# Kernel optimization log

Measured on AMD Instinct MI355X. Metric: run time of the kernel, lower is better.

The kernel has to match this reference:

```python
import jax, jax.numpy as jnp
import numpy as np

N_NODES = 100_000
N_EDGES = 6_400_000  # avg degree 64
ONE_THIRD = 1.0 / 3.0


def _safe_cbrt(x):
    # x >= 0 by construction (relu upstream); guard x==0 so pow grad stays finite.
    pos = x > 0
    xs = jnp.where(pos, x, 1.0)
    return jnp.where(pos, xs ** ONE_THIRD, 0.0)


def setup_inputs() -> dict:
    key = jax.random.key(0)
    ks = jax.random.split(key, 8)
    T = jax.random.uniform(ks[0], (N_NODES,), jnp.float32, 1.8, 4.5)          # node temperature [K]
    cp = jax.random.uniform(ks[1], (N_NODES,), jnp.float32, 0.5, 2.0)         # node thermal capacity
    L = jax.random.uniform(ks[2], (N_EDGES,), jnp.float32, 0.1, 2.0)          # edge length (>0)
    conductivity = jax.random.uniform(ks[3], (N_EDGES,), jnp.float32, 0.5, 1.5)
    A = jax.random.uniform(ks[4], (N_EDGES,), jnp.float32, 0.01, 1.0)         # cross-section area
    src = jax.random.randint(ks[5], (N_EDGES,), 0, N_NODES, jnp.int32)
    dst = jax.random.randint(ks[6], (N_EDGES,), 0, N_NODES, jnp.int32)
    time_step = jnp.full((1,), 0.1, jnp.float32)                              # context scalar
    return {"T": T, "cp": cp, "L": L, "conductivity": conductivity, "A": A,
            "time_step": time_step, "src": src, "dst": dst}


def reference(T, cp, L, conductivity, A, time_step, src, dst):
    n = T.shape[0]
    # broadcast node -> edge; relu(-(T_target - T_source)) == relu(T_src - T_dst)
    delta_T = jax.nn.relu(T[src] - T[dst])                 # [E]
    gradient_T = delta_T / L                               # [E]
    heat_flux_density = _safe_cbrt(gradient_T * conductivity)
    heat_flux = heat_flux_density * A
    E_transf_conduction = heat_flux * time_step            # broadcast [1]
    cp_s = cp[src]
    cp_t = cp[dst]
    combined_cp = cp_t * cp_s / (cp_t + cp_s)
    max_energy = delta_T * combined_cp
    E_transf = jnp.minimum(E_transf_conduction, max_energy)
    heat_sent = jax.ops.segment_sum(E_transf, src, num_segments=n)
    heat_received = jax.ops.segment_sum(E_transf, dst, num_segments=n)
    return heat_received - heat_sent                       # [N]
```

## Files before the change

### kernel.cpp

```cpp
#include <hip/hip_runtime.h>
#include <hip/hip_bf16.h>
#include <hip/hip_fp16.h>

#define NRANGE   8
#define RLEN_MAX 12800
#define N_XCD    8
#define SL_XCD   8
#define SLICES   64
#define WIN_E    2048

typedef float vfloat4 __attribute__((ext_vector_type(4)));
typedef unsigned long long u64;

__global__ void __launch_bounds__(256)
pack_nodes_kernel(const float* __restrict__ T, const float* __restrict__ cp,
                  float2* __restrict__ nodes, int* __restrict__ tails, int n) {
    int i = blockIdx.x * blockDim.x + threadIdx.x;
    if (i < n) nodes[i] = make_float2(T[i], cp[i]);
    if (blockIdx.x == 0 && threadIdx.x < SLICES) tails[threadIdx.x] = 0;
}

__device__ __forceinline__ float edge_e(float2 ns, float2 nd, float Li,
                                        float ci, float Ai, float dt) {
    const float delta = ns.x - nd.x;
    if (delta <= 0.0f) return 0.0f;
    const float x = (delta / Li) * ci;
    const float ec = cbrtf(x) * Ai * dt;
    const float comb = (nd.y * ns.y) / (nd.y + ns.y);
    return fminf(ec, delta * comb);
}

__device__ __forceinline__ u64 make_rec(int s, int d, float e) {
    return (u64)(unsigned)s | ((u64)(unsigned)d << 17)
         | ((u64)__half_as_ushort(__float2half_rn(e)) << 34);
}

__global__ void __launch_bounds__(512)
etrec_kernel(const float2* __restrict__ nodes,
             const float* __restrict__ L,
             const float* __restrict__ cond,
             const float* __restrict__ A,
             const float* __restrict__ time_step,
             const int* __restrict__ src,
             const int* __restrict__ dst,
             u64* __restrict__ recs,
             int* __restrict__ tails,
             int n_edges, int wps, int cap) {
    __shared__ u64 srec[8 * 256];
    __shared__ int wcnt[8];
    __shared__ int wbase[8];
    __shared__ int sbase;

    const int wpx  = SL_XCD * wps;
    const int w    = (blockIdx.x % N_XCD) * wpx + blockIdx.x / N_XCD;
    const int s    = w / wps;
    const int e0   = w * WIN_E;
    const int wave = threadIdx.x >> 6;
    const int lane = threadIdx.x & 63;

    int my_off = 0;
    const bool active = (e0 < n_edges);

    if (active) {
        const float dt = time_step[0];
        float ev[4]; int sv[4]; int dv[4];

        if (e0 + WIN_E <= n_edges) {
            const int kk = (e0 >> 2) + threadIdx.x;
            const int4    si = ((const int4*)src)[kk];
            const int4    di = ((const int4*)dst)[kk];
            const vfloat4 Lv = __builtin_nontemporal_load(&((const vfloat4*)L)[kk]);
            const vfloat4 cv = __builtin_nontemporal_load(&((const vfloat4*)cond)[kk]);
            const vfloat4 Av = __builtin_nontemporal_load(&((const vfloat4*)A)[kk]);
            const float2 ns0 = nodes[si.x], ns1 = nodes[si.y], ns2 = nodes[si.z], ns3 = nodes[si.w];
            const float2 nd0 = nodes[di.x], nd1 = nodes[di.y], nd2 = nodes[di.z], nd3 = nodes[di.w];
            ev[0] = edge_e(ns0, nd0, Lv.x, cv.x, Av.x, dt);
            ev[1] = edge_e(ns1, nd1, Lv.y, cv.y, Av.y, dt);
            ev[2] = edge_e(ns2, nd2, Lv.z, cv.z, Av.z, dt);
            ev[3] = edge_e(ns3, nd3, Lv.w, cv.w, Av.w, dt);
            sv[0] = si.x; sv[1] = si.y; sv[2] = si.z; sv[3] = si.w;
            dv[0] = di.x; dv[1] = di.y; dv[2] = di.z; dv[3] = di.w;
        } else {
#pragma unroll
            for (int j = 0; j < 4; ++j) {
                const int i = e0 + 4 * (int)threadIdx.x + j;
                float e = 0.0f; int a = 0, b2 = 0;
                if (i < n_edges) {
                    a = src[i]; b2 = dst[i];
                    e = edge_e(nodes[a], nodes[b2], L[i], cond[i], A[i], dt);
                }
                ev[j] = e; sv[j] = a; dv[j] = b2;
            }
        }

#pragma unroll
        for (int j = 0; j < 4; ++j) {
            const u64 mask = __ballot(ev[j] > 0.0f);
            if (ev[j] > 0.0f) {
                const int pos = my_off + __popcll(mask & ((1ull << lane) - 1ull));
                srec[(wave << 8) + pos] = make_rec(sv[j], dv[j], ev[j]);
            }
            my_off += (int)__popcll(mask);
        }
    }

    if (lane == 0) wcnt[wave] = my_off;
    __syncthreads();
    if (threadIdx.x == 0) {
        int tot = 0;
#pragma unroll
        for (int i = 0; i < 8; ++i) { wbase[i] = tot; tot += wcnt[i]; }
        sbase = (tot > 0) ? atomicAdd(&tails[s], tot) : 0;
    }
    __syncthreads();

    if (active) {
        const int c  = wcnt[wave];
        const int gb = sbase + wbase[wave];
        u64* __restrict__ dp = recs + (size_t)s * cap;
        for (int t = lane; t < c; t += 64) {
            const int p = gb + t;
            if (p < cap) dp[p] = srec[(wave << 8) + t];
        }
    }
}

__device__ __forceinline__ void acc_rec(u64 rec, float* __restrict__ lds,
                                        int base, int rlen) {
    const int   sv = (int)(rec & 0x1FFFF);
    const int   dv = (int)((rec >> 17) & 0x1FFFF);
    const float e  = __half2float(__ushort_as_half((unsigned short)(rec >> 34)));
    const int ls = sv - base; if ((unsigned)ls < (unsigned)rlen) atomicAdd(&lds[ls], -e);
    const int ld = dv - base; if ((unsigned)ld < (unsigned)rlen) atomicAdd(&lds[ld],  e);
}

__global__ void __launch_bounds__(512)
accrec_kernel(const u64* __restrict__ recs,
              const int* __restrict__ tails,
              float* __restrict__ copies,
              int n_nodes, int R, int cap) {
    __shared__ float lds[RLEN_MAX];
    const int xcd = blockIdx.x % N_XCD;
    const int j   = blockIdx.x / N_XCD;
    const int r   = j % NRANGE;
    const int b   = xcd * SL_XCD + j / NRANGE;
    const int base = r * R;
    const int rlen = min(R, n_nodes - base);

    for (int t = threadIdx.x; t < rlen; t += 512) lds[t] = 0.0f;
    __syncthreads();

    const int cnt = min(tails[b], cap);
    const u64* __restrict__ g = recs + (size_t)b * cap;
    const int npair = cnt >> 1;
    const ulonglong2* __restrict__ g2 = (const ulonglong2*)g;
    for (int t = threadIdx.x; t < npair; t += 1024) {
        const int t2 = t + 512;
        const bool h2 = (t2 < npair);
        const ulonglong2 r0 = g2[t];
        ulonglong2 r1;
        if (h2) r1 = g2[t2];
        acc_rec(r0.x, lds, base, rlen);
        acc_rec(r0.y, lds, base, rlen);
        if (h2) {
            acc_rec(r1.x, lds, base, rlen);
            acc_rec(r1.y, lds, base, rlen);
        }
    }
    for (int t = (npair << 1) + (int)threadIdx.x; t < cnt; t += 512)
        acc_rec(g[t], lds, base, rlen);
    __syncthreads();

    float* __restrict__ cpy = copies + (size_t)b * n_nodes + base;
    for (int t = threadIdx.x; t < rlen; t += 512) cpy[t] = lds[t];
}

__global__ void __launch_bounds__(256)
reduce_copies_kernel(const float* __restrict__ copies, float* __restrict__ out,
                     int n_nodes) {
    const int k = blockIdx.x * blockDim.x + threadIdx.x;
    const int nvec = n_nodes >> 2;
    if (k < nvec) {
        vfloat4 v = {0.f, 0.f, 0.f, 0.f};
        for (int b = 0; b < SLICES; ++b)
            v += ((const vfloat4*)(copies + (size_t)b * n_nodes))[k];
        ((vfloat4*)out)[k] = v;
    } else if (k == nvec) {
        for (int i = nvec << 2; i < n_nodes; ++i) {
            float v = 0.0f;
            for (int b = 0; b < SLICES; ++b) v += copies[(size_t)b * n_nodes + i];
            out[i] = v;
        }
    }
}

__global__ void __launch_bounds__(256)
conduction_edge_direct(const float* __restrict__ T, const float* __restrict__ cp,
                       const float* __restrict__ L, const float* __restrict__ cond,
                       const float* __restrict__ A, const float* __restrict__ time_step,
                       const int* __restrict__ src, const int* __restrict__ dst,
                       float* __restrict__ out, int n_edges) {
    int i = blockIdx.x * blockDim.x + threadIdx.x;
    if (i >= n_edges) return;
    const int s = src[i], d = dst[i];
    float delta = T[s] - T[d];
    if (delta <= 0.0f) return;
    const float dt = time_step[0];
    const float x = (delta / L[i]) * cond[i];
    const float e_cond = cbrtf(x) * A[i] * dt;
    const float cs = cp[s], cd = cp[d];
    const float max_e = delta * (cd * cs) / (cd + cs);
    const float Et = fminf(e_cond, max_e);
    atomicAdd(&out[d],  Et);
    atomicAdd(&out[s], -Et);
}

extern "C" void kernel_launch(void* const* d_in, const int* in_sizes, int n_in,
                              void* d_out, int out_size, void* d_ws, size_t ws_size,
                              hipStream_t stream) {
    const float* T    = (const float*)d_in[0];
    const float* cp   = (const float*)d_in[1];
    const float* L    = (const float*)d_in[2];
    const float* cond = (const float*)d_in[3];
    const float* A    = (const float*)d_in[4];
    const float* ts   = (const float*)d_in[5];
    const int*   src  = (const int*)d_in[6];
    const int*   dst  = (const int*)d_in[7];
    float* out = (float*)d_out;

    const int n_nodes = in_sizes[0];
    const int n_edges = in_sizes[2];

    const int block = 256;
    const int ngrid = (n_nodes + block - 1) / block;
    const int R = (n_nodes + NRANGE - 1) / NRANGE;

    int chunk = (n_edges + SLICES - 1) / SLICES;
    chunk = (chunk + WIN_E - 1) & ~(WIN_E - 1);
    const int wps = chunk / WIN_E;
    const int cap = (chunk >> 3) * 5;

    const size_t tails_bytes = 256;
    const size_t nodes_bytes = (size_t)n_nodes * sizeof(float2);
    const size_t recs_bytes  = (size_t)SLICES * cap * sizeof(u64);
    const size_t copy_bytes  = (size_t)SLICES * n_nodes * sizeof(float);
    const size_t need = tails_bytes + nodes_bytes + recs_bytes + copy_bytes;

    if (R <= RLEN_MAX && n_nodes <= (1 << 17) && ws_size >= need) {
        int*    tails  = (int*)d_ws;
        float2* nodes  = (float2*)((char*)d_ws + tails_bytes);
        u64*    recs   = (u64*)((char*)d_ws + tails_bytes + nodes_bytes);
        float*  copies = (float*)((char*)d_ws + tails_bytes + nodes_bytes + recs_bytes);

        pack_nodes_kernel<<<ngrid, block, 0, stream>>>(T, cp, nodes, tails, n_nodes);
        etrec_kernel<<<SLICES * wps, 512, 0, stream>>>(
            nodes, L, cond, A, ts, src, dst, recs, tails, n_edges, wps, cap);
        accrec_kernel<<<N_XCD * SL_XCD * NRANGE, 512, 0, stream>>>(
            recs, tails, copies, n_nodes, R, cap);
        const int rgrid = ((n_nodes >> 2) + 1 + block - 1) / block;
        reduce_copies_kernel<<<rgrid, block, 0, stream>>>(copies, out, n_nodes);
    } else {
        (void)hipMemsetAsync(out, 0, (size_t)out_size * sizeof(float), stream);
        const int egrid = (n_edges + block - 1) / block;
        conduction_edge_direct<<<egrid, block, 0, stream>>>(
            T, cp, L, cond, A, ts, src, dst, out, n_edges);
    }
}
```

Baseline: 247.1 us.

## Widen LDS node ranges, use 1024-thread accumulation blocks, split reduction by XCD group

The accumulation kernel now covers each slice with 4 node ranges of up to 25600 nodes instead of 8 smaller ones. Blocks grow to 1024 threads, each loading four record pairs per iteration. This halves how often each slice's record stream is re-read, at the cost of more LDS per block and lower occupancy. The final reduction is split into 8 groups per XCD that atomically add partial sums into an output zeroed in the pack kernel, which brings float atomics and makes summation order nondeterministic.

Result: slower. 253.7 us (+2.7%).

```diff
diff --git a/kernel.cpp b/kernel.cpp
--- a/kernel.cpp
+++ b/kernel.cpp
@@ -2,8 +2,8 @@
 #include <hip/hip_bf16.h>
 #include <hip/hip_fp16.h>
 
-#define NRANGE   8
-#define RLEN_MAX 12800
+#define NRANGE   4
+#define RLEN_MAX 25600
 #define N_XCD    8
 #define SL_XCD   8
 #define SLICES   64
@@ -14,9 +14,13 @@
 
 __global__ void __launch_bounds__(256)
 pack_nodes_kernel(const float* __restrict__ T, const float* __restrict__ cp,
-                  float2* __restrict__ nodes, int* __restrict__ tails, int n) {
+                  float2* __restrict__ nodes, int* __restrict__ tails,
+                  float* __restrict__ out, int n) {
     int i = blockIdx.x * blockDim.x + threadIdx.x;
-    if (i < n) nodes[i] = make_float2(T[i], cp[i]);
+    if (i < n) {
+        nodes[i] = make_float2(T[i], cp[i]);
+        out[i] = 0.0f;
+    }
     if (blockIdx.x == 0 && threadIdx.x < SLICES) tails[threadIdx.x] = 0;
 }
 
@@ -134,7 +138,7 @@
     const int ld = dv - base; if ((unsigned)ld < (unsigned)rlen) atomicAdd(&lds[ld],  e);
 }
 
-__global__ void __launch_bounds__(512)
+__global__ void __launch_bounds__(1024)
 accrec_kernel(const u64* __restrict__ recs,
               const int* __restrict__ tails,
               float* __restrict__ copies,
@@ -146,50 +150,64 @@
     const int b   = xcd * SL_XCD + j / NRANGE;
     const int base = r * R;
     const int rlen = min(R, n_nodes - base);
-
-    for (int t = threadIdx.x; t < rlen; t += 512) lds[t] = 0.0f;
+    if (rlen <= 0) return;
+
+    for (int t = threadIdx.x; t < rlen; t += 1024) lds[t] = 0.0f;
     __syncthreads();
 
     const int cnt = min(tails[b], cap);
     const u64* __restrict__ g = recs + (size_t)b * cap;
     const int npair = cnt >> 1;
     const ulonglong2* __restrict__ g2 = (const ulonglong2*)g;
-    for (int t = threadIdx.x; t < npair; t += 1024) {
-        const int t2 = t + 512;
-        const bool h2 = (t2 < npair);
+    for (int t = threadIdx.x; t < npair; t += 4096) {
+        const int tmax = npair - 1;
+        const int tb = min(t + 1024, tmax);
+        const int tc = min(t + 2048, tmax);
+        const int td = min(t + 3072, tmax);
+        const bool hb = (t + 1024 < npair);
+        const bool hc = (t + 2048 < npair);
+        const bool hd = (t + 3072 < npair);
         const ulonglong2 r0 = g2[t];
-        ulonglong2 r1;
-        if (h2) r1 = g2[t2];
+        const ulonglong2 r1 = g2[tb];
+        const ulonglong2 r2 = g2[tc];
+        const ulonglong2 r3 = g2[td];
         acc_rec(r0.x, lds, base, rlen);
         acc_rec(r0.y, lds, base, rlen);
-        if (h2) {
-            acc_rec(r1.x, lds, base, rlen);
-            acc_rec(r1.y, lds, base, rlen);
-        }
-    }
-    for (int t = (npair << 1) + (int)threadIdx.x; t < cnt; t += 512)
+        if (hb) { acc_rec(r1.x, lds, base, rlen); acc_rec(r1.y, lds, base, rlen); }
+        if (hc) { acc_rec(r2.x, lds, base, rlen); acc_rec(r2.y, lds, base, rlen); }
+        if (hd) { acc_rec(r3.x, lds, base, rlen); acc_rec(r3.y, lds, base, rlen); }
+    }
+    for (int t = (npair << 1) + (int)threadIdx.x; t < cnt; t += 1024)
         acc_rec(g[t], lds, base, rlen);
     __syncthreads();
 
     float* __restrict__ cpy = copies + (size_t)b * n_nodes + base;
-    for (int t = threadIdx.x; t < rlen; t += 512) cpy[t] = lds[t];
+    for (int t = threadIdx.x; t < rlen; t += 1024) cpy[t] = lds[t];
 }
 
 __global__ void __launch_bounds__(256)
-reduce_copies_kernel(const float* __restrict__ copies, float* __restrict__ out,
+reduce_groups_kernel(const float* __restrict__ copies, float* __restrict__ out,
                      int n_nodes) {
-    const int k = blockIdx.x * blockDim.x + threadIdx.x;
+    const int bg = blockIdx.x % N_XCD;
+    const int kb = blockIdx.x / N_XCD;
+    const int k  = kb * 256 + (int)threadIdx.x;
     const int nvec = n_nodes >> 2;
+    const float* __restrict__ base = copies + (size_t)bg * SL_XCD * n_nodes;
     if (k < nvec) {
         vfloat4 v = {0.f, 0.f, 0.f, 0.f};
-        for (int b = 0; b < SLICES; ++b)
-            v += ((const vfloat4*)(copies + (size_t)b * n_nodes))[k];
-        ((vfloat4*)out)[k] = v;
+#pragma unroll
+        for (int s = 0; s < SL_XCD; ++s)
+            v += ((const vfloat4*)(base + (size_t)s * n_nodes))[k];
+        float* o = out + ((size_t)k << 2);
+        atomicAdd(&o[0], v.x);
+        atomicAdd(&o[1], v.y);
+        atomicAdd(&o[2], v.z);
+        atomicAdd(&o[3], v.w);
     } else if (k == nvec) {
         for (int i = nvec << 2; i < n_nodes; ++i) {
             float v = 0.0f;
-            for (int b = 0; b < SLICES; ++b) v += copies[(size_t)b * n_nodes + i];
-            out[i] = v;
+            for (int s = 0; s < SL_XCD; ++s) v += base[(size_t)s * n_nodes + i];
+            atomicAdd(&out[i], v);
         }
     }
 }
@@ -252,13 +270,13 @@
         u64*    recs   = (u64*)((char*)d_ws + tails_bytes + nodes_bytes);
         float*  copies = (float*)((char*)d_ws + tails_bytes + nodes_bytes + recs_bytes);
 
-        pack_nodes_kernel<<<ngrid, block, 0, stream>>>(T, cp, nodes, tails, n_nodes);
+        pack_nodes_kernel<<<ngrid, block, 0, stream>>>(T, cp, nodes, tails, out, n_nodes);
         etrec_kernel<<<SLICES * wps, 512, 0, stream>>>(
             nodes, L, cond, A, ts, src, dst, recs, tails, n_edges, wps, cap);
-        accrec_kernel<<<N_XCD * SL_XCD * NRANGE, 512, 0, stream>>>(
+        accrec_kernel<<<N_XCD * SL_XCD * NRANGE, 1024, 0, stream>>>(
             recs, tails, copies, n_nodes, R, cap);
-        const int rgrid = ((n_nodes >> 2) + 1 + block - 1) / block;
-        reduce_copies_kernel<<<rgrid, block, 0, stream>>>(copies, out, n_nodes);
+        const int rblocks = ((n_nodes >> 2) + 1 + 255) / 256;
+        reduce_groups_kernel<<<N_XCD * rblocks, 256, 0, stream>>>(copies, out, n_nodes);
     } else {
         (void)hipMemsetAsync(out, 0, (size_t)out_size * sizeof(float), stream);
         const int egrid = (n_edges + block - 1) / block;
```

## Fuse four pipeline kernels into one cooperative kernel with grid syncs

Applied to the files above, without the earlier changes.

Replaces the pack, edge-record, per-slice accumulate and copy-reduce launches with a single cooperative kernel of 512 blocks that loops over the old work items and separates the phases with grid.sync. The shared-memory buffers of the record and accumulate phases share one union. The aim is to remove launch gaps and kernel tail drain between stages. In exchange each phase now runs on a fixed grid and pays grid-wide barrier costs, and the edge phase loops over many windows per block. If the cooperative launch fails, the original four-kernel path runs instead.

New measurement: 715.6 us. +189.6%, slower.

```diff
diff --git a/kernel.cpp b/kernel.cpp
--- a/kernel.cpp
+++ b/kernel.cpp
@@ -1,6 +1,9 @@
 #include <hip/hip_runtime.h>
 #include <hip/hip_bf16.h>
 #include <hip/hip_fp16.h>
+#include <hip/hip_cooperative_groups.h>
+
+namespace cg = cooperative_groups;
 
 #define NRANGE   8
 #define RLEN_MAX 12800
@@ -8,17 +11,11 @@
 #define SL_XCD   8
 #define SLICES   64
 #define WIN_E    2048
+#define FB       512
+#define FT       512
 
 typedef float vfloat4 __attribute__((ext_vector_type(4)));
 typedef unsigned long long u64;
-
-__global__ void __launch_bounds__(256)
-pack_nodes_kernel(const float* __restrict__ T, const float* __restrict__ cp,
-                  float2* __restrict__ nodes, int* __restrict__ tails, int n) {
-    int i = blockIdx.x * blockDim.x + threadIdx.x;
-    if (i < n) nodes[i] = make_float2(T[i], cp[i]);
-    if (blockIdx.x == 0 && threadIdx.x < SLICES) tails[threadIdx.x] = 0;
-}
 
 __device__ __forceinline__ float edge_e(float2 ns, float2 nd, float Li,
                                         float ci, float Ai, float dt) {
@@ -35,6 +32,181 @@
          | ((u64)__half_as_ushort(__float2half_rn(e)) << 34);
 }
 
+__device__ __forceinline__ void acc_rec(u64 rec, float* __restrict__ lds,
+                                        int base, int rlen) {
+    const int   sv = (int)(rec & 0x1FFFF);
+    const int   dv = (int)((rec >> 17) & 0x1FFFF);
+    const float e  = __half2float(__ushort_as_half((unsigned short)(rec >> 34)));
+    const int ls = sv - base; if ((unsigned)ls < (unsigned)rlen) atomicAdd(&lds[ls], -e);
+    const int ld = dv - base; if ((unsigned)ld < (unsigned)rlen) atomicAdd(&lds[ld],  e);
+}
+
+__global__ void __launch_bounds__(FT, 4)
+fused_kernel(const float* __restrict__ T, const float* __restrict__ cp,
+             const float* __restrict__ L, const float* __restrict__ cond,
+             const float* __restrict__ A, const float* __restrict__ time_step,
+             const int* __restrict__ src, const int* __restrict__ dst,
+             float2* __restrict__ nodes, u64* __restrict__ recs,
+             int* __restrict__ tails, float* __restrict__ copies,
+             float* __restrict__ out,
+             int n_nodes, int n_edges, int wps, int cap, int R) {
+    cg::grid_group grid = cg::this_grid();
+    __shared__ union SH {
+        struct { u64 srec[8 * 256]; int wcnt[8]; int wbase[8]; int sbase; } e;
+        float acc[RLEN_MAX];
+    } sh;
+
+    const int b   = blockIdx.x;
+    const int tid = threadIdx.x;
+
+    for (int i = b * FT + tid; i < n_nodes; i += FB * FT)
+        nodes[i] = make_float2(T[i], cp[i]);
+    if (b == 0 && tid < SLICES) tails[tid] = 0;
+    __threadfence();
+    grid.sync();
+
+    {
+        const float dt  = time_step[0];
+        const int wave  = tid >> 6;
+        const int lane  = tid & 63;
+        const int wpx   = SL_XCD * wps;
+        const int nwin  = SLICES * wps;
+        for (int vb = b; vb < nwin; vb += FB) {
+            const int w  = (vb % N_XCD) * wpx + vb / N_XCD;
+            const int s  = w / wps;
+            const int e0 = w * WIN_E;
+            int my_off = 0;
+            const bool active = (e0 < n_edges);
+
+            if (active) {
+                float ev[4]; int sv[4]; int dv[4];
+                if (e0 + WIN_E <= n_edges) {
+                    const int kk = (e0 >> 2) + tid;
+                    const int4    si = ((const int4*)src)[kk];
+                    const int4    di = ((const int4*)dst)[kk];
+                    const vfloat4 Lv = __builtin_nontemporal_load(&((const vfloat4*)L)[kk]);
+                    const vfloat4 cv = __builtin_nontemporal_load(&((const vfloat4*)cond)[kk]);
+                    const vfloat4 Av = __builtin_nontemporal_load(&((const vfloat4*)A)[kk]);
+                    const float2 ns0 = nodes[si.x], ns1 = nodes[si.y], ns2 = nodes[si.z], ns3 = nodes[si.w];
+                    const float2 nd0 = nodes[di.x], nd1 = nodes[di.y], nd2 = nodes[di.z], nd3 = nodes[di.w];
+                    ev[0] = edge_e(ns0, nd0, Lv.x, cv.x, Av.x, dt);
+                    ev[1] = edge_e(ns1, nd1, Lv.y, cv.y, Av.y, dt);
+                    ev[2] = edge_e(ns2, nd2, Lv.z, cv.z, Av.z, dt);
+                    ev[3] = edge_e(ns3, nd3, Lv.w, cv.w, Av.w, dt);
+                    sv[0] = si.x; sv[1] = si.y; sv[2] = si.z; sv[3] = si.w;
+                    dv[0] = di.x; dv[1] = di.y; dv[2] = di.z; dv[3] = di.w;
+                } else {
+#pragma unroll
+                    for (int j = 0; j < 4; ++j) {
+                        const int i = e0 + 4 * tid + j;
+                        float e = 0.0f; int a = 0, b2 = 0;
+                        if (i < n_edges) {
+                            a = src[i]; b2 = dst[i];
+                            e = edge_e(nodes[a], nodes[b2], L[i], cond[i], A[i], dt);
+                        }
+                        ev[j] = e; sv[j] = a; dv[j] = b2;
+                    }
+                }
+#pragma unroll
+                for (int j = 0; j < 4; ++j) {
+                    const u64 mask = __ballot(ev[j] > 0.0f);
+                    if (ev[j] > 0.0f) {
+                        const int pos = my_off + __popcll(mask & ((1ull << lane) - 1ull));
+                        sh.e.srec[(wave << 8) + pos] = make_rec(sv[j], dv[j], ev[j]);
+                    }
+                    my_off += (int)__popcll(mask);
+                }
+            }
+
+            if (lane == 0) sh.e.wcnt[wave] = my_off;
+            __syncthreads();
+            if (tid == 0) {
+                int tot = 0;
+#pragma unroll
+                for (int i = 0; i < 8; ++i) { sh.e.wbase[i] = tot; tot += sh.e.wcnt[i]; }
+                sh.e.sbase = (tot > 0) ? atomicAdd(&tails[s], tot) : 0;
+            }
+            __syncthreads();
+
+            if (active) {
+                const int c  = sh.e.wcnt[wave];
+                const int gb = sh.e.sbase + sh.e.wbase[wave];
+                u64* __restrict__ dp = recs + (size_t)s * cap;
+                for (int t = lane; t < c; t += 64) {
+                    const int p = gb + t;
+                    if (p < cap) dp[p] = sh.e.srec[(wave << 8) + t];
+                }
+            }
+            __syncthreads();
+        }
+    }
+    __threadfence();
+    grid.sync();
+
+    {
+        const int xcd  = b % N_XCD;
+        const int j    = b / N_XCD;
+        const int r    = j % NRANGE;
+        const int sl   = xcd * SL_XCD + j / NRANGE;
+        const int base = r * R;
+        const int rlen = min(R, n_nodes - base);
+        if (rlen > 0) {
+            for (int t = tid; t < rlen; t += FT) sh.acc[t] = 0.0f;
+            __syncthreads();
+
+            const int cnt = min(tails[sl], cap);
+            const u64* __restrict__ g = recs + (size_t)sl * cap;
+            const int npair = cnt >> 1;
+            const ulonglong2* __restrict__ g2 = (const ulonglong2*)g;
+            for (int t = tid; t < npair; t += 2 * FT) {
+                const int t2 = t + FT;
+                const bool h2 = (t2 < npair);
+                const ulonglong2 r0 = g2[t];
+                ulonglong2 r1;
+                if (h2) r1 = g2[t2];
+                acc_rec(r0.x, sh.acc, base, rlen);
+                acc_rec(r0.y, sh.acc, base, rlen);
+                if (h2) { acc_rec(r1.x, sh.acc, base, rlen); acc_rec(r1.y, sh.acc, base, rlen); }
+            }
+            for (int t = (npair << 1) + tid; t < cnt; t += FT)
+                acc_rec(g[t], sh.acc, base, rlen);
+            __syncthreads();
+
+            float* __restrict__ cpy = copies + (size_t)sl * n_nodes + base;
+            for (int t = tid; t < rlen; t += FT) cpy[t] = sh.acc[t];
+        }
+    }
+    __threadfence();
+    grid.sync();
+
+    {
+        const int nvec = n_nodes >> 2;
+        for (int k = b * FT + tid; k <= nvec; k += FB * FT) {
+            if (k < nvec) {
+                vfloat4 v = {0.f, 0.f, 0.f, 0.f};
+#pragma unroll 8
+                for (int s2 = 0; s2 < SLICES; ++s2)
+                    v += ((const vfloat4*)(copies + (size_t)s2 * n_nodes))[k];
+                ((vfloat4*)out)[k] = v;
+            } else {
+                for (int i = nvec << 2; i < n_nodes; ++i) {
+                    float v = 0.0f;
+                    for (int s2 = 0; s2 < SLICES; ++s2) v += copies[(size_t)s2 * n_nodes + i];
+                    out[i] = v;
+                }
+            }
+        }
+    }
+}
+
+__global__ void __launch_bounds__(256)
+pack_nodes_kernel(const float* __restrict__ T, const float* __restrict__ cp,
+                  float2* __restrict__ nodes, int* __restrict__ tails, int n) {
+    int i = blockIdx.x * blockDim.x + threadIdx.x;
+    if (i < n) nodes[i] = make_float2(T[i], cp[i]);
+    if (blockIdx.x == 0 && threadIdx.x < SLICES) tails[threadIdx.x] = 0;
+}
+
 __global__ void __launch_bounds__(512)
 etrec_kernel(const float2* __restrict__ nodes,
              const float* __restrict__ L,
@@ -43,8 +215,7 @@
              const float* __restrict__ time_step,
              const int* __restrict__ src,
              const int* __restrict__ dst,
-             u64* __restrict__ recs,
-             int* __restrict__ tails,
+             u64* __restrict__ recs, int* __restrict__ tails,
              int n_edges, int wps, int cap) {
     __shared__ u64 srec[8 * 256];
     __shared__ int wcnt[8];
@@ -64,7 +235,6 @@
     if (active) {
         const float dt = time_step[0];
         float ev[4]; int sv[4]; int dv[4];
-
         if (e0 + WIN_E <= n_edges) {
             const int kk = (e0 >> 2) + threadIdx.x;
             const int4    si = ((const int4*)src)[kk];
@@ -92,7 +262,6 @@
                 ev[j] = e; sv[j] = a; dv[j] = b2;
             }
         }
-
 #pragma unroll
         for (int j = 0; j < 4; ++j) {
             const u64 mask = __ballot(ev[j] > 0.0f);
@@ -123,15 +292,6 @@
             if (p < cap) dp[p] = srec[(wave << 8) + t];
         }
     }
-}
-
-__device__ __forceinline__ void acc_rec(u64 rec, float* __restrict__ lds,
-                                        int base, int rlen) {
-    const int   sv = (int)(rec & 0x1FFFF);
-    const int   dv = (int)((rec >> 17) & 0x1FFFF);
-    const float e  = __half2float(__ushort_as_half((unsigned short)(rec >> 34)));
-    const int ls = sv - base; if ((unsigned)ls < (unsigned)rlen) atomicAdd(&lds[ls], -e);
-    const int ld = dv - base; if ((unsigned)ld < (unsigned)rlen) atomicAdd(&lds[ld],  e);
 }
 
 __global__ void __launch_bounds__(512)
@@ -146,6 +306,7 @@
     const int b   = xcd * SL_XCD + j / NRANGE;
     const int base = r * R;
     const int rlen = min(R, n_nodes - base);
+    if (rlen <= 0) return;
 
     for (int t = threadIdx.x; t < rlen; t += 512) lds[t] = 0.0f;
     __syncthreads();
@@ -162,10 +323,7 @@
         if (h2) r1 = g2[t2];
         acc_rec(r0.x, lds, base, rlen);
         acc_rec(r0.y, lds, base, rlen);
-        if (h2) {
-            acc_rec(r1.x, lds, base, rlen);
-            acc_rec(r1.y, lds, base, rlen);
-        }
+        if (h2) { acc_rec(r1.x, lds, base, rlen); acc_rec(r1.y, lds, base, rlen); }
     }
     for (int t = (npair << 1) + (int)threadIdx.x; t < cnt; t += 512)
         acc_rec(g[t], lds, base, rlen);
@@ -228,17 +386,17 @@
     const int*   dst  = (const int*)d_in[7];
     float* out = (float*)d_out;
 
-    const int n_nodes = in_sizes[0];
-    const int n_edges = in_sizes[2];
+    int n_nodes = in_sizes[0];
+    int n_edges = in_sizes[2];
 
     const int block = 256;
     const int ngrid = (n_nodes + block - 1) / block;
-    const int R = (n_nodes + NRANGE - 1) / NRANGE;
+    int R = (n_nodes + NRANGE - 1) / NRANGE;
 
     int chunk = (n_edges + SLICES - 1) / SLICES;
     chunk = (chunk + WIN_E - 1) & ~(WIN_E - 1);
-    const int wps = chunk / WIN_E;
-    const int cap = (chunk >> 3) * 5;
+    int wps = chunk / WIN_E;
+    int cap = (chunk >> 3) * 5;
 
     const size_t tails_bytes = 256;
     const size_t nodes_bytes = (size_t)n_nodes * sizeof(float2);
@@ -252,13 +410,25 @@
         u64*    recs   = (u64*)((char*)d_ws + tails_bytes + nodes_bytes);
         float*  copies = (float*)((char*)d_ws + tails_bytes + nodes_bytes + recs_bytes);
 
-        pack_nodes_kernel<<<ngrid, block, 0, stream>>>(T, cp, nodes, tails, n_nodes);
-        etrec_kernel<<<SLICES * wps, 512, 0, stream>>>(
-            nodes, L, cond, A, ts, src, dst, recs, tails, n_edges, wps, cap);
-        accrec_kernel<<<N_XCD * SL_XCD * NRANGE, 512, 0, stream>>>(
-            recs, tails, copies, n_nodes, R, cap);
-        const int rgrid = ((n_nodes >> 2) + 1 + block - 1) / block;
-        reduce_copies_kernel<<<rgrid, block, 0, stream>>>(copies, out, n_nodes);
+        void* kargs[] = {
+            (void*)&T, (void*)&cp, (void*)&L, (void*)&cond, (void*)&A, (void*)&ts,
+            (void*)&src, (void*)&dst, (void*)&nodes, (void*)&recs, (void*)&tails,
+            (void*)&copies, (void*)&out,
+            (void*)&n_nodes, (void*)&n_edges, (void*)&wps, (void*)&cap, (void*)&R };
+
+        hipError_t err = hipLaunchCooperativeKernel(
+            (const void*)fused_kernel, dim3(FB), dim3(FT), kargs, 0, stream);
+
+        if (err != hipSuccess) {
+            (void)hipGetLastError();
+            pack_nodes_kernel<<<ngrid, block, 0, stream>>>(T, cp, nodes, tails, n_nodes);
+            etrec_kernel<<<SLICES * wps, 512, 0, stream>>>(
+                nodes, L, cond, A, ts, src, dst, recs, tails, n_edges, wps, cap);
+            accrec_kernel<<<N_XCD * SL_XCD * NRANGE, 512, 0, stream>>>(
+                recs, tails, copies, n_nodes, R, cap);
+            const int rgrid = ((n_nodes >> 2) + 1 + block - 1) / block;
+            reduce_copies_kernel<<<rgrid, block, 0, stream>>>(copies, out, n_nodes);
+        }
     } else {
         (void)hipMemsetAsync(out, 0, (size_t)out_size * sizeof(float), stream);
         const int egrid = (n_edges + block - 1) / block;
```
